# Optimization experiments

Measured on AMD Instinct MI355X. Metric: run time of the kernel, lower is better.

Reference implementation:

```python
import jax, jax.numpy as jnp
import numpy as np

HEADS = 8
DIM_HEAD = 64
SCALE = DIM_HEAD ** -0.5


def setup_inputs() -> dict:
    key = jax.random.key(0)
    k1, k2, k3 = jax.random.split(key, 3)
    B, C, L = 4, 512, 2048
    h_dim = HEADS * DIM_HEAD  # 512
    x = jax.random.normal(k1, (B, C, L), dtype=jnp.float32)
    w_qkv = jax.random.normal(k2, (C, 3 * h_dim), dtype=jnp.float32) * (C ** -0.5)
    w_out = jax.random.normal(k3, (h_dim, C), dtype=jnp.float32) * (h_dim ** -0.5)
    b_out = jnp.zeros((C,), dtype=jnp.float32)
    return {"x": x, "w_qkv": w_qkv, "w_out": w_out, "b_out": b_out}


def reference(x, w_qkv, w_out, b_out):
    B, C, L = x.shape
    # pointwise conv (kernel size 1, no bias): [B,C,L] x [C,3hd] -> [B,3hd,L]
    qkv = jnp.einsum('bcl,cf->bfl', x, w_qkv)
    q, k, v = jnp.split(qkv, 3, axis=1)  # each [B, h*d, L]
    def to_heads(t):
        return t.reshape(B, HEADS, DIM_HEAD, L)  # b h d l
    q, k, v = to_heads(q), to_heads(k), to_heads(v)
    q = q * SCALE
    sim = jnp.einsum('bhdi,bhdj->bhij', q, k)  # [B,H,L,L]
    attn = jax.nn.softmax(sim, axis=-1)  # stable (max-subtract) softmax
    out = jnp.einsum('bhij,bhdj->bhid', attn, v)  # [B,H,L,D]
    # rearrange 'b h l c -> b (h c) l'
    out = out.transpose(0, 1, 3, 2).reshape(B, HEADS * DIM_HEAD, L)
    # to_out pointwise conv with bias: [B,hd,L] -> [B,C,L]
    return jnp.einsum('bcl,cf->bfl', out, w_out) + b_out[None, :, None]
```

## Files before the change

### kernel.cpp

```cpp
#include <hip/hip_runtime.h>


#define LDIM 2048
#define CDIM 512
#define BATCH 4

typedef __attribute__((ext_vector_type(8))) short s16x8;
typedef __attribute__((ext_vector_type(4))) float f32x4;
typedef __attribute__((ext_vector_type(4))) unsigned short u16x4;
typedef unsigned int u32;
typedef unsigned short u16;

__device__ __forceinline__ u16 f2b(float f) {
    unsigned u = __float_as_uint(f);
    u += 0x7fffu + ((u >> 16) & 1u);
    return (u16)(u >> 16);
}
__device__ __forceinline__ u32 pk2(float a, float b) {
    u32 ua = __float_as_uint(a) + 0x8000u;
    u32 ub = __float_as_uint(b) + 0x8000u;
    return __builtin_amdgcn_perm(ub, ua, 0x07060302u);
}

__global__ __launch_bounds__(256)
void transpA_k(const float* __restrict__ x, const float* __restrict__ wq,
               const float* __restrict__ wo, u16* __restrict__ XP,
               u16* __restrict__ WP, u16* __restrict__ WOP)
{
    const int r0 = blockIdx.x * 64;
    const int y  = blockIdx.y;
    const float* in; u16* out; int inLD, c0;
    if (y < 128) {
        const int b = y >> 5, ct = y & 31;
        in = x + (size_t)b * CDIM * LDIM; inLD = LDIM; c0 = ct * 64;
        out = XP + (size_t)b * LDIM * CDIM;
    } else if (y < 152) {
        in = wq; inLD = 1536; c0 = (y - 128) * 64; out = WP;
    } else {
        in = wo; inLD = 512;  c0 = (y - 152) * 64; out = WOP;
    }

    __shared__ __align__(16) u16 t[64][80];
    const int tt = threadIdx.x;
    const int lr = tt >> 4, lc = (tt & 15) * 4;
    #pragma unroll
    for (int i = 0; i < 4; ++i) {
        f32x4 v = *(const f32x4*)(in + (size_t)(r0 + lr + i * 16) * inLD + c0 + lc);
        #pragma unroll
        for (int j = 0; j < 4; ++j) t[lc + j][lr + i * 16] = f2b(v[j]);
    }
    __syncthreads();
    const int orow = tt >> 2, ocg = (tt & 3) * 16;
    s16x8 v0 = *(const s16x8*)&t[orow][ocg];
    s16x8 v1 = *(const s16x8*)&t[orow][ocg + 8];
    const int row   = c0 + orow;
    const int rtile = row >> 4, rr = row & 15;
    const int cstep = (r0 + ocg) >> 5;
    const int qb    = (ocg >> 3) & 3;
    u16* dst = out + ((size_t)(rtile * 16 + cstep) * 64 + qb * 16 + rr) * 8;
    *(s16x8*)dst = v0;
    *(s16x8*)(dst + 128) = v1;
}

__global__ __launch_bounds__(256)
void qkvgemm_bf16(const u16* __restrict__ XP, const u16* __restrict__ WP,
                  u16* __restrict__ QF, u16* __restrict__ KF, u16* __restrict__ VF)
{
    const int f0 = blockIdx.x * 64;
    const int l0 = blockIdx.y * 128;
    const int b  = blockIdx.z;
    const u16* xTb = XP + (size_t)b * LDIM * CDIM;
    const int t = threadIdx.x, w = t >> 6, lane = t & 63;
    const int mn = lane & 15, q = lane >> 4;
    const bool vpart = (f0 >= 1024);

    const u16 *Abase, *Bbase;
    int mbase, nbase;
    if (!vpart) {
        mbase = f0 + (w >> 1) * 32; nbase = l0 + (w & 1) * 64;
        Abase = WP + (size_t)mbase * CDIM; Bbase = xTb + (size_t)nbase * CDIM;
    } else {
        mbase = l0 + w * 32; nbase = f0;
        Abase = xTb + (size_t)mbase * CDIM; Bbase = WP + (size_t)nbase * CDIM;
    }

    f32x4 acc[2][4] = {};
    #pragma unroll 2
    for (int c0 = 0; c0 < CDIM; c0 += 32) {
        s16x8 a[2], bf[4];
        #pragma unroll
        for (int mi = 0; mi < 2; ++mi)
            a[mi] = *(const s16x8*)(Abase + mi * 16 * CDIM + c0 * 16 + lane * 8);
        #pragma unroll
        for (int ni = 0; ni < 4; ++ni)
            bf[ni] = *(const s16x8*)(Bbase + ni * 16 * CDIM + c0 * 16 + lane * 8);
        #pragma unroll
        for (int mi = 0; mi < 2; ++mi)
            #pragma unroll
            for (int ni = 0; ni < 4; ++ni)
                acc[mi][ni] = __builtin_amdgcn_mfma_f32_16x16x32_bf16(a[mi], bf[ni], acc[mi][ni], 0, 0, 0);
    }

    if (!vpart) {
        const int part = f0 >> 9;
        const float sc2 = (part == 0) ? 0.18033688f : 1.0f;
        u16* Tout = (part == 0) ? QF : KF;
        #pragma unroll
        for (int mi = 0; mi < 2; ++mi) {
            const int fg0 = mbase + mi * 16;
            const int h = (fg0 >> 6) & 7;
            const int d0 = (fg0 & 63) + q * 4;
            const int kd = d0 >> 5, qq = (d0 >> 3) & 3, e0 = d0 & 7;
            u16* T = Tout + (size_t)(b * 8 + h) * LDIM * 64;
            #pragma unroll
            for (int ni = 0; ni < 4; ++ni) {
                const int lg = nbase + ni * 16 + mn;
                size_t addr;
                if (part == 0) {
                    const int t16 = lg >> 4, mnq = lg & 15;
                    addr = (size_t)((t16 * 2 + kd) * 512 + (qq * 16 + mnq) * 8 + e0);
                } else {
                    const int j64 = lg >> 6, r6 = lg & 63;
                    const int jt  = ((r6 >> 2) & 1) * 2 + (r6 >> 5);
                    const int mnk = ((r6 >> 3) & 3) * 4 + (r6 & 3);
                    addr = (size_t)(((j64 * 4 + jt) * 2 + kd) * 512 + (qq * 16 + mnk) * 8 + e0);
                }
                u16x4 pk;
                #pragma unroll
                for (int r = 0; r < 4; ++r) pk[r] = f2b(acc[mi][ni][r] * sc2);
                *(u16x4*)(T + addr) = pk;
            }
        }
    } else {
        #pragma unroll
        for (int ni = 0; ni < 4; ++ni) {
            const int fg = nbase + ni * 16 + mn;
            const int h = (fg >> 6) & 7;
            const int d = fg & 63;
            const int dt = d >> 4, mnv = d & 15;
            u16* Vb = VF + (size_t)(b * 8 + h) * LDIM * 64;
            #pragma unroll
            for (int mi = 0; mi < 2; ++mi) {
                const int lg0 = mbase + mi * 16 + q * 4;
                const int j64 = lg0 >> 6, j6 = lg0 & 63;
                const int kj = j6 >> 5, qq = (j6 >> 3) & 3, e0 = j6 & 7;
                const size_t addr = (size_t)(((j64 * 2 + kj) * 4 + dt) * 512 + (qq * 16 + mnv) * 8 + e0);
                u16x4 pk;
                #pragma unroll
                for (int r = 0; r < 4; ++r) pk[r] = f2b(acc[mi][ni][r]);
                *(u16x4*)(Vb + addr) = pk;
            }
        }
    }
}

__global__ __launch_bounds__(128)
void attn_k(const u16* __restrict__ QF, const u16* __restrict__ KF,
            const u16* __restrict__ VF, u16* __restrict__ aoP)
{
    const int bh = blockIdx.x;
    const int b = bh >> 3, h = bh & 7;
    const u16* Qh = QF + (size_t)bh * LDIM * 64;
    const u16* Kh = KF + (size_t)bh * LDIM * 64;
    const u16* Vh = VF + (size_t)bh * LDIM * 64;

    __shared__ __align__(16) float o_sh[64][68];
    __shared__ float lp_sh[64];

    const int tid = threadIdx.x;
    const int wv = tid >> 6;
    const int lane = tid & 63;
    const int mn = lane & 15, q = lane >> 4;
    const int ib64 = blockIdx.y;
    const int TH = 16;
    const int tbase = wv * TH;

    s16x8 aq[4][2];
    #pragma unroll
    for (int ibt = 0; ibt < 4; ++ibt) {
        const int t16 = ib64 * 4 + ibt;
        #pragma unroll
        for (int kd = 0; kd < 2; ++kd)
            aq[ibt][kd] = *(const s16x8*)(Qh + (size_t)((t16 * 2 + kd) * 512) + lane * 8);
    }

    f32x4 o_acc[4][4] = {};
    float lp[4] = {0.f, 0.f, 0.f, 0.f};

    s16x8 kc[2][4], vc[2][4];
    {
        const u16* Kt = Kh + (size_t)tbase * 4096;
        const u16* Vt = Vh + (size_t)tbase * 4096;
        #pragma unroll
        for (int kd = 0; kd < 2; ++kd)
            #pragma unroll
            for (int jt = 0; jt < 4; ++jt)
                kc[kd][jt] = *(const s16x8*)(Kt + ((jt * 2 + kd) << 9) + (lane << 3));
        #pragma unroll
        for (int kj = 0; kj < 2; ++kj)
            #pragma unroll
            for (int dt = 0; dt < 4; ++dt)
                vc[kj][dt] = *(const s16x8*)(Vt + ((kj * 4 + dt) << 9) + (lane << 3));
    }

    #pragma unroll 2
    for (int jj = 0; jj < TH; ++jj) {
        const int tn = tbase + ((jj + 1) & (TH - 1));
        const u16* Kt = Kh + (size_t)tn * 4096;
        const u16* Vt = Vh + (size_t)tn * 4096;

        s16x8 kn[2][4];
        #pragma unroll
        for (int kd = 0; kd < 2; ++kd)
            #pragma unroll
            for (int jt = 0; jt < 4; ++jt)
                kn[kd][jt] = *(const s16x8*)(Kt + ((jt * 2 + kd) << 9) + (lane << 3));

        f32x4 s[4][4] = {};
        #pragma unroll
        for (int kd = 0; kd < 2; ++kd)
            #pragma unroll
            for (int jt = 0; jt < 4; ++jt)
                #pragma unroll
                for (int ibt = 0; ibt < 4; ++ibt)
                    s[ibt][jt] = __builtin_amdgcn_mfma_f32_16x16x32_bf16(kc[kd][jt], aq[ibt][kd], s[ibt][jt], 0, 0, 0);

        s16x8 vn[2][4];
        #pragma unroll
        for (int kj = 0; kj < 2; ++kj)
            #pragma unroll
            for (int dt = 0; dt < 4; ++dt)
                vn[kj][dt] = *(const s16x8*)(Vt + ((kj * 4 + dt) << 9) + (lane << 3));

        #pragma unroll
        for (int kj = 0; kj < 2; ++kj) {
            s16x8 ap[4];
            #pragma unroll
            for (int ibt = 0; ibt < 4; ++ibt) {
                float pa0 = __builtin_amdgcn_exp2f(s[ibt][kj][0]);
                float pa1 = __builtin_amdgcn_exp2f(s[ibt][kj][1]);
                float pa2 = __builtin_amdgcn_exp2f(s[ibt][kj][2]);
                float pa3 = __builtin_amdgcn_exp2f(s[ibt][kj][3]);
                float pb0 = __builtin_amdgcn_exp2f(s[ibt][kj + 2][0]);
                float pb1 = __builtin_amdgcn_exp2f(s[ibt][kj + 2][1]);
                float pb2 = __builtin_amdgcn_exp2f(s[ibt][kj + 2][2]);
                float pb3 = __builtin_amdgcn_exp2f(s[ibt][kj + 2][3]);
                lp[ibt] += ((pa0 + pa1) + (pa2 + pa3)) + ((pb0 + pb1) + (pb2 + pb3));
                union { s16x8 v; u32 w[4]; } u;
                u.w[0] = pk2(pa0, pa1);
                u.w[1] = pk2(pa2, pa3);
                u.w[2] = pk2(pb0, pb1);
                u.w[3] = pk2(pb2, pb3);
                ap[ibt] = u.v;
            }
            #pragma unroll
            for (int dt = 0; dt < 4; ++dt)
                #pragma unroll
                for (int ibt = 0; ibt < 4; ++ibt)
                    o_acc[ibt][dt] = __builtin_amdgcn_mfma_f32_16x16x32_bf16(vc[kj][dt], ap[ibt], o_acc[ibt][dt], 0, 0, 0);
        }

        #pragma unroll
        for (int kd = 0; kd < 2; ++kd)
            #pragma unroll
            for (int jt = 0; jt < 4; ++jt)
                kc[kd][jt] = kn[kd][jt];
        #pragma unroll
        for (int kj = 0; kj < 2; ++kj)
            #pragma unroll
            for (int dt = 0; dt < 4; ++dt)
                vc[kj][dt] = vn[kj][dt];
    }

    #pragma unroll
    for (int ibt = 0; ibt < 4; ++ibt) {
        lp[ibt] += __shfl_xor(lp[ibt], 16);
        lp[ibt] += __shfl_xor(lp[ibt], 32);
    }

    if (wv == 1) {
        #pragma unroll
        for (int ibt = 0; ibt < 4; ++ibt) {
            #pragma unroll
            for (int dt = 0; dt < 4; ++dt)
                *(f32x4*)&o_sh[ibt * 16 + mn][dt * 16 + q * 4] = o_acc[ibt][dt];
            if (q == 0) lp_sh[ibt * 16 + mn] = lp[ibt];
        }
    }
    __syncthreads();
    if (wv == 0) {
        u16* Ab = aoP + (size_t)b * LDIM * 512;
        #pragma unroll
        for (int ibt = 0; ibt < 4; ++ibt) {
            const float rinv = 1.0f / (lp[ibt] + lp_sh[ibt * 16 + mn]);
            const int ltile = ib64 * 4 + ibt;
            #pragma unroll
            for (int dt = 0; dt < 4; ++dt) {
                f32x4 os = *(const f32x4*)&o_sh[ibt * 16 + mn][dt * 16 + q * 4];
                u16x4 pk;
                #pragma unroll
                for (int r = 0; r < 4; ++r)
                    pk[r] = f2b((o_acc[ibt][dt][r] + os[r]) * rinv);
                const int cstep = h * 2 + (dt >> 1);
                const int lanep = ((dt & 1) * 2 + (q >> 1)) * 16 + mn;
                u16* dst = Ab + ((size_t)(ltile * 16 + cstep) * 64 + lanep) * 8 + (q & 1) * 4;
                *(u16x4*)dst = pk;
            }
        }
    }
}

__global__ __launch_bounds__(256)
void outgemm_d(const u16* __restrict__ aoP, const u16* __restrict__ WOP,
               const float* __restrict__ bias, float* __restrict__ Y)
{
    const int f0 = blockIdx.x * 64;
    const int l0 = blockIdx.y * 128;
    const int b  = blockIdx.z;
    const int t = threadIdx.x, w = t >> 6, lane = t & 63;
    const int mn = lane & 15, q = lane >> 4;
    const int mbase = f0 + (w >> 1) * 32;
    const int nbase = l0 + (w & 1) * 64;
    const u16* Abase = WOP + (size_t)mbase * CDIM;
    const u16* Bbase = aoP + ((size_t)b * LDIM + nbase) * CDIM;
    float* Yb = Y + (size_t)b * CDIM * LDIM;

    f32x4 acc[2][4] = {};
    #pragma unroll 2
    for (int c0 = 0; c0 < CDIM; c0 += 32) {
        s16x8 a[2], bf[4];
        #pragma unroll
        for (int mi = 0; mi < 2; ++mi)
            a[mi] = *(const s16x8*)(Abase + mi * 16 * CDIM + c0 * 16 + lane * 8);
        #pragma unroll
        for (int ni = 0; ni < 4; ++ni)
            bf[ni] = *(const s16x8*)(Bbase + ni * 16 * CDIM + c0 * 16 + lane * 8);
        #pragma unroll
        for (int mi = 0; mi < 2; ++mi)
            #pragma unroll
            for (int ni = 0; ni < 4; ++ni)
                acc[mi][ni] = __builtin_amdgcn_mfma_f32_16x16x32_bf16(a[mi], bf[ni], acc[mi][ni], 0, 0, 0);
    }
    #pragma unroll
    for (int mi = 0; mi < 2; ++mi)
        #pragma unroll
        for (int r = 0; r < 4; ++r) {
            const int f = mbase + mi * 16 + q * 4 + r;
            const float bs = bias[f];
            #pragma unroll
            for (int ni = 0; ni < 4; ++ni)
                Yb[(size_t)f * LDIM + nbase + ni * 16 + mn] = acc[mi][ni][r] + bs;
        }
}

extern "C" void kernel_launch(void* const* d_in, const int* in_sizes, int n_in,
                              void* d_out, int out_size, void* d_ws, size_t ws_size,
                              hipStream_t stream) {
    const float *x = nullptr, *w_qkv = nullptr, *w_out = nullptr, *b_out = nullptr;
    for (int i = 0; i < n_in; ++i) {
        switch (in_sizes[i]) {
            case 4 * 512 * 2048: x     = (const float*)d_in[i]; break;
            case 512 * 1536:     w_qkv = (const float*)d_in[i]; break;
            case 512 * 512:      w_out = (const float*)d_in[i]; break;
            case 512:            b_out = (const float*)d_in[i]; break;
        }
    }
    float* out = (float*)d_out;

    const size_t SLAB = (size_t)BATCH * LDIM * 512;
    u16* WOP = (u16*)d_ws;
    u16* XP  = WOP + (size_t)512 * 512;
    u16* WP  = XP + SLAB;
    u16* QF  = WP + (size_t)1536 * 512;
    u16* KF  = QF + SLAB;
    u16* VF  = KF + SLAB;
    u16* aoP = VF + SLAB;

    transpA_k<<<dim3(8, 160), 256, 0, stream>>>(x, w_qkv, w_out, XP, WP, WOP);
    qkvgemm_bf16<<<dim3(24, 16, BATCH), 256, 0, stream>>>(XP, WP, QF, KF, VF);
    attn_k<<<dim3(32, 32), 128, 0, stream>>>(QF, KF, VF, aoP);
    outgemm_d<<<dim3(8, 16, BATCH), 256, 0, stream>>>(aoP, WOP, b_out, out);
}
```

Measured before the change: 176.7 us.

## Split attention key range across four waves and drop V register prefetch

The attention kernel now launches 256 threads (four waves) per block. Each wave handles 8 key tiles instead of 16, and the partial outputs and row sums are reduced through a three-slot shared buffer. V tiles are now loaded within the current iteration rather than prefetched one iteration ahead, which cuts register pressure so that launch_bounds(256,3) can be met. This adds more waves to hide latency, at the cost of a larger LDS reduction and V loads that are no longer overlapped.

```diff
diff --git a/kernel.cpp b/kernel.cpp
--- a/kernel.cpp
+++ b/kernel.cpp
@@ -154,7 +154,7 @@
     }
 }
 
-__global__ __launch_bounds__(128)
+__global__ __launch_bounds__(256, 3)
 void attn_k(const u16* __restrict__ QF, const u16* __restrict__ KF,
             const u16* __restrict__ VF, u16* __restrict__ aoP)
 {
@@ -164,15 +164,15 @@
     const u16* Kh = KF + (size_t)bh * LDIM * 64;
     const u16* Vh = VF + (size_t)bh * LDIM * 64;
 
-    __shared__ __align__(16) float o_sh[64][68];
-    __shared__ float lp_sh[64];
+    __shared__ __align__(16) float o_sh[3][64][68];
+    __shared__ float lp_sh[3][64];
 
     const int tid = threadIdx.x;
     const int wv = tid >> 6;
     const int lane = tid & 63;
     const int mn = lane & 15, q = lane >> 4;
     const int ib64 = blockIdx.y;
-    const int TH = 16;
+    const int TH = 8;
     const int tbase = wv * TH;
 
     s16x8 aq[4][2];
@@ -187,27 +187,21 @@
     f32x4 o_acc[4][4] = {};
     float lp[4] = {0.f, 0.f, 0.f, 0.f};
 
-    s16x8 kc[2][4], vc[2][4];
+    s16x8 kc[2][4];
     {
         const u16* Kt = Kh + (size_t)tbase * 4096;
-        const u16* Vt = Vh + (size_t)tbase * 4096;
         #pragma unroll
         for (int kd = 0; kd < 2; ++kd)
             #pragma unroll
             for (int jt = 0; jt < 4; ++jt)
                 kc[kd][jt] = *(const s16x8*)(Kt + ((jt * 2 + kd) << 9) + (lane << 3));
-        #pragma unroll
-        for (int kj = 0; kj < 2; ++kj)
-            #pragma unroll
-            for (int dt = 0; dt < 4; ++dt)
-                vc[kj][dt] = *(const s16x8*)(Vt + ((kj * 4 + dt) << 9) + (lane << 3));
     }
 
     #pragma unroll 2
     for (int jj = 0; jj < TH; ++jj) {
         const int tn = tbase + ((jj + 1) & (TH - 1));
         const u16* Kt = Kh + (size_t)tn * 4096;
-        const u16* Vt = Vh + (size_t)tn * 4096;
+        const u16* Vt = Vh + (size_t)(tbase + jj) * 4096;
 
         s16x8 kn[2][4];
         #pragma unroll
@@ -225,12 +219,12 @@
                 for (int ibt = 0; ibt < 4; ++ibt)
                     s[ibt][jt] = __builtin_amdgcn_mfma_f32_16x16x32_bf16(kc[kd][jt], aq[ibt][kd], s[ibt][jt], 0, 0, 0);
 
-        s16x8 vn[2][4];
+        s16x8 vc[2][4];
         #pragma unroll
         for (int kj = 0; kj < 2; ++kj)
             #pragma unroll
             for (int dt = 0; dt < 4; ++dt)
-                vn[kj][dt] = *(const s16x8*)(Vt + ((kj * 4 + dt) << 9) + (lane << 3));
+                vc[kj][dt] = *(const s16x8*)(Vt + ((kj * 4 + dt) << 9) + (lane << 3));
 
         #pragma unroll
         for (int kj = 0; kj < 2; ++kj) {
@@ -265,11 +259,6 @@
             #pragma unroll
             for (int jt = 0; jt < 4; ++jt)
                 kc[kd][jt] = kn[kd][jt];
-        #pragma unroll
-        for (int kj = 0; kj < 2; ++kj)
-            #pragma unroll
-            for (int dt = 0; dt < 4; ++dt)
-                vc[kj][dt] = vn[kj][dt];
     }
 
     #pragma unroll
@@ -278,13 +267,13 @@
         lp[ibt] += __shfl_xor(lp[ibt], 32);
     }
 
-    if (wv == 1) {
+    if (wv != 0) {
         #pragma unroll
         for (int ibt = 0; ibt < 4; ++ibt) {
             #pragma unroll
             for (int dt = 0; dt < 4; ++dt)
-                *(f32x4*)&o_sh[ibt * 16 + mn][dt * 16 + q * 4] = o_acc[ibt][dt];
-            if (q == 0) lp_sh[ibt * 16 + mn] = lp[ibt];
+                *(f32x4*)&o_sh[wv - 1][ibt * 16 + mn][dt * 16 + q * 4] = o_acc[ibt][dt];
+            if (q == 0) lp_sh[wv - 1][ibt * 16 + mn] = lp[ibt];
         }
     }
     __syncthreads();
@@ -292,15 +281,19 @@
         u16* Ab = aoP + (size_t)b * LDIM * 512;
         #pragma unroll
         for (int ibt = 0; ibt < 4; ++ibt) {
-            const float rinv = 1.0f / (lp[ibt] + lp_sh[ibt * 16 + mn]);
+            const int row = ibt * 16 + mn;
+            const float lptot = lp[ibt] + lp_sh[0][row] + lp_sh[1][row] + lp_sh[2][row];
+            const float rinv = 1.0f / lptot;
             const int ltile = ib64 * 4 + ibt;
             #pragma unroll
             for (int dt = 0; dt < 4; ++dt) {
-                f32x4 os = *(const f32x4*)&o_sh[ibt * 16 + mn][dt * 16 + q * 4];
+                f32x4 o0 = *(const f32x4*)&o_sh[0][row][dt * 16 + q * 4];
+                f32x4 o1 = *(const f32x4*)&o_sh[1][row][dt * 16 + q * 4];
+                f32x4 o2 = *(const f32x4*)&o_sh[2][row][dt * 16 + q * 4];
                 u16x4 pk;
                 #pragma unroll
                 for (int r = 0; r < 4; ++r)
-                    pk[r] = f2b((o_acc[ibt][dt][r] + os[r]) * rinv);
+                    pk[r] = f2b((o_acc[ibt][dt][r] + o0[r] + o1[r] + o2[r]) * rinv);
                 const int cstep = h * 2 + (dt >> 1);
                 const int lanep = ((dt & 1) * 2 + (q >> 1)) * 16 + mn;
                 u16* dst = Ab + ((size_t)(ltile * 16 + cstep) * 64 + lanep) * 8 + (q & 1) * 4;
@@ -378,6 +371,6 @@
 
     transpA_k<<<dim3(8, 160), 256, 0, stream>>>(x, w_qkv, w_out, XP, WP, WOP);
     qkvgemm_bf16<<<dim3(24, 16, BATCH), 256, 0, stream>>>(XP, WP, QF, KF, VF);
-    attn_k<<<dim3(32, 32), 128, 0, stream>>>(QF, KF, VF, aoP);
+    attn_k<<<dim3(32, 32), 256, 0, stream>>>(QF, KF, VF, aoP);
     outgemm_d<<<dim3(8, 16, BATCH), 256, 0, stream>>>(aoP, WOP, b_out, out);
 }
```

Measured after the change: 302.2 us. 1.71x slower.
